# Kernel tuning notes

Measured on AMD Instinct MI355X. Metric: run time of the kernel, lower is better.

## Reference

```python
import jax, jax.numpy as jnp
import numpy as np

B, S, D_MODEL, D_QK = 4, 4096, 256, 64


def setup_inputs() -> dict:
    key = jax.random.key(0)
    ks = jax.random.split(key, 6)
    enc_q = jax.random.normal(ks[0], (B, S, D_MODEL), dtype=jnp.float32)
    enc_k = jax.random.normal(ks[1], (B, S, D_MODEL), dtype=jnp.float32)
    enc_v = jax.random.normal(ks[2], (B, S, D_MODEL), dtype=jnp.float32)
    # torch nn.Linear weight layout: [out_features, in_features]
    Wq = jax.random.normal(ks[3], (D_QK, D_MODEL), dtype=jnp.float32) * (D_MODEL ** -0.5)
    Wk = jax.random.normal(ks[4], (D_QK, D_MODEL), dtype=jnp.float32) * (D_MODEL ** -0.5)
    Wv = jax.random.normal(ks[5], (D_MODEL, D_MODEL), dtype=jnp.float32) * (D_MODEL ** -0.5)
    # causal mask: True above the diagonal -> masked out (matches masked_fill semantics)
    mask = jnp.triu(jnp.ones((S, S), dtype=jnp.bool_), k=1)
    return {"encodings_for_q": enc_q, "encodings_for_k": enc_k,
            "encodings_for_v": enc_v, "mask": mask,
            "Wq": Wq, "Wk": Wk, "Wv": Wv}


def reference(encodings_for_q, encodings_for_k, encodings_for_v, mask, Wq, Wk, Wv):
    # linear projections (no bias): x @ W.T
    q = jnp.einsum('bsd,qd->bsq', encodings_for_q, Wq)   # [B,S,d_qk]
    k = jnp.einsum('bsd,qd->bsq', encodings_for_k, Wk)   # [B,S,d_qk]
    v = jnp.einsum('bsd,ed->bse', encodings_for_v, Wv)   # [B,S,d_model]
    scale = k.shape[-1] ** 0.5                            # sqrt(d_qk)
    sims = jnp.einsum('bsq,btq->bst', q, k) / scale       # [B,S,S]
    sims = jnp.where(mask, jnp.float32(-1e9), sims)
    attn = jax.nn.softmax(sims, axis=-1)
    return jnp.einsum('bst,bte->bse', attn, v)            # [B,S,d_model]
```

## Files before the change

kernel.cpp:

```cpp
#include <hip/hip_runtime.h>


#define BATCH 4
#define SEQ   4096
#define DM    256
#define DQK   64

typedef __bf16 bf16x8 __attribute__((ext_vector_type(8)));
typedef float  f32x16 __attribute__((ext_vector_type(16)));

__device__ __forceinline__ unsigned int rnd16(unsigned int u) {
    return u + 0x7fffu + ((u >> 16) & 1u);
}
__device__ __forceinline__ unsigned short f2bf(float f) {
    return (unsigned short)(rnd16(__builtin_bit_cast(unsigned int, f)) >> 16);
}
__device__ __forceinline__ unsigned int pk2bf(float lo, float hi) {
    unsigned int a = rnd16(__builtin_bit_cast(unsigned int, lo));
    unsigned int b = rnd16(__builtin_bit_cast(unsigned int, hi));
    return (a >> 16) | (b & 0xffff0000u);
}
__device__ __forceinline__ bf16x8 u4bf(uint4 u) { return __builtin_bit_cast(bf16x8, u); }

__device__ __forceinline__ void repack_store(const f32x16& acc, int q2, int l,
                                             uint4* __restrict__ out, size_t tile_ofs_u4) {
    unsigned int d0[4], d1[4], p0[4], p1[4];
#pragma unroll
    for (int h = 0; h < 4; ++h) {
        d0[h] = pk2bf(acc[4*h + 0], acc[4*h + 1]);
        d1[h] = pk2bf(acc[4*h + 2], acc[4*h + 3]);
        p0[h] = __shfl_xor((int)d0[h], 32);
        p1[h] = __shfl_xor((int)d1[h], 32);
    }
#pragma unroll
    for (int kc = 0; kc < 2; ++kc) {
        int h = 2*kc + q2;
        uint4 v = (q2 == 0) ? make_uint4(d0[h], d1[h], p0[h], p1[h])
                            : make_uint4(p0[h], p1[h], d0[h], d1[h]);
        out[tile_ofs_u4 + (size_t)kc * 64 + l] = v;
    }
}

__global__ __launch_bounds__(256) void proj(const float* __restrict__ Xq,
                                            const float* __restrict__ Xk,
                                            const float* __restrict__ Xv,
                                            const float* __restrict__ Wq,
                                            const float* __restrict__ Wk,
                                            const float* __restrict__ Wv,
                                            uint4* __restrict__ qf,
                                            uint4* __restrict__ kf,
                                            uint4* __restrict__ vf) {
    __shared__ unsigned short Xs[64][264];
    __shared__ unsigned short Ws[64][264];

    const int z = blockIdx.z;
    const int bx = blockIdx.x, b = blockIdx.y;
    const float* X = (z == 0) ? Xq : (z == 1) ? Xk : Xv;
    const float* W = (z == 0) ? Wq : (z == 1) ? Wk : Wv;
    const int s0 = bx * 64;
    const int tid = threadIdx.x, w = tid >> 6, l = tid & 63, ln = l & 31, q2 = l >> 5;

#pragma unroll
    for (int i = 0; i < 16; ++i) {
        int f = i * 256 + tid;
        int r = f >> 6, c4 = f & 63;
        float4 xv = *(const float4*)&X[((size_t)b * SEQ + s0 + r) * DM + c4 * 4];
        ushort4 h; h.x = f2bf(xv.x); h.y = f2bf(xv.y); h.z = f2bf(xv.z); h.w = f2bf(xv.w);
        *(ushort4*)&Xs[r][c4 * 4] = h;
    }

    if (z < 2) {
#pragma unroll
        for (int i = 0; i < 16; ++i) {
            int f = i * 256 + tid;
            int r = f >> 6, c4 = f & 63;
            float4 wv = *(const float4*)&W[(size_t)r * DM + c4 * 4];
            ushort4 h; h.x = f2bf(wv.x); h.y = f2bf(wv.y); h.z = f2bf(wv.z); h.w = f2bf(wv.w);
            *(ushort4*)&Ws[r][c4 * 4] = h;
        }
        __syncthreads();
        const int msub = w >> 1, nsub = w & 1;
        f32x16 a0 = {}, a1 = {};
#pragma unroll
        for (int c = 0; c < 16; c += 2) {
            bf16x8 af0 = u4bf(*(const uint4*)&Ws[msub*32 + ln][c*16 + q2*8]);
            bf16x8 bf0 = u4bf(*(const uint4*)&Xs[nsub*32 + ln][c*16 + q2*8]);
            a0 = __builtin_amdgcn_mfma_f32_32x32x16_bf16(af0, bf0, a0, 0, 0, 0);
            bf16x8 af1 = u4bf(*(const uint4*)&Ws[msub*32 + ln][(c+1)*16 + q2*8]);
            bf16x8 bf1 = u4bf(*(const uint4*)&Xs[nsub*32 + ln][(c+1)*16 + q2*8]);
            a1 = __builtin_amdgcn_mfma_f32_32x32x16_bf16(af1, bf1, a1, 0, 0, 0);
        }
        f32x16 acc = a0 + a1;
        size_t base = (((size_t)(b*128 + bx*2 + nsub)) * 4 + 2*msub) * 64;
        repack_store(acc, q2, l, (z == 0) ? qf : kf, base);
    } else {
        const int msub = w & 1, nsub = w >> 1;
        for (int ec = 0; ec < 4; ++ec) {
            __syncthreads();
#pragma unroll
            for (int i = 0; i < 16; ++i) {
                int f = i * 256 + tid;
                int r = f >> 6, c4 = f & 63;
                float4 wv = *(const float4*)&W[(size_t)(ec*64 + r) * DM + c4 * 4];
                ushort4 h; h.x = f2bf(wv.x); h.y = f2bf(wv.y); h.z = f2bf(wv.z); h.w = f2bf(wv.w);
                *(ushort4*)&Ws[r][c4 * 4] = h;
            }
            __syncthreads();
            f32x16 a0 = {}, a1 = {};
#pragma unroll
            for (int c = 0; c < 16; c += 2) {
                bf16x8 af0 = u4bf(*(const uint4*)&Xs[msub*32 + ln][c*16 + q2*8]);
                bf16x8 bf0 = u4bf(*(const uint4*)&Ws[nsub*32 + ln][c*16 + q2*8]);
                a0 = __builtin_amdgcn_mfma_f32_32x32x16_bf16(af0, bf0, a0, 0, 0, 0);
                bf16x8 af1 = u4bf(*(const uint4*)&Xs[msub*32 + ln][(c+1)*16 + q2*8]);
                bf16x8 bf1 = u4bf(*(const uint4*)&Ws[nsub*32 + ln][(c+1)*16 + q2*8]);
                a1 = __builtin_amdgcn_mfma_f32_32x32x16_bf16(af1, bf1, a1, 0, 0, 0);
            }
            f32x16 acc = a0 + a1;
            int et = ec*2 + nsub;
            size_t base = (((size_t)(b*8 + et)) * 256 + (size_t)bx*4 + msub*2) * 64;
            repack_store(acc, q2, l, vf, base);
        }
    }
}

__global__ __launch_bounds__(512) void attn(const uint4* __restrict__ qf,
                                            const uint4* __restrict__ kf,
                                            const uint4* __restrict__ vf,
                                            float* __restrict__ out,
                                            unsigned short* __restrict__ Op,
                                            float* __restrict__ Dp) {
    __shared__ uint4 Pb[2][4][8][64];
    __shared__ float denp[8][2][64];
    __shared__ float dfin[128];

    const int bid = blockIdx.x;
    const int slot = bid & 7, u = bid >> 3;
    const int b = slot >> 1;
    const int task = u * 2 + (slot & 1);
    int T, cc, nc;
    if (task < 12)      { T = task;                cc = 0;             nc = 1; }
    else if (task < 36) { int q = task - 12; T = 12 + (q >> 1); cc = q & 1;     nc = 2; }
    else                { int q = task - 36; T = 24 + q / 3;    cc = q - 3*(q/3); nc = 3; }
    const int n = T + 1;
    const int j0 = cc * n / nc, j1 = (cc + 1) * n / nc;

    const int tid = threadIdx.x, w = tid >> 6, l = tid & 63, ln = l & 31, q2 = l >> 5;
    const int ks = w & 3, qp = w >> 2;
    const float cfac = 0.18033688011112042f;

    bf16x8 qv[2][4];
#pragma unroll
    for (int g = 0; g < 2; ++g)
#pragma unroll
        for (int c = 0; c < 4; ++c)
            qv[g][c] = u4bf(qf[(((size_t)b*128 + T*4 + qp*2 + g) * 4 + c) * 64 + l]);

    f32x16 oa[4] = {};
    float den[2] = {0.f, 0.f};

    uint4 kaf[4];
#pragma unroll
    for (int c = 0; c < 4; ++c)
        kaf[c] = kf[(((size_t)b*128 + j0*4 + ks) * 4 + c) * 64 + l];

    for (int jt = j0; jt < j1; ++jt) {
        const int buf = jt & 1;
        const bool diag = (jt == T);
        f32x16 s0 = {}, s1 = {};
#pragma unroll
        for (int c = 0; c < 4; ++c) {
            bf16x8 ka = u4bf(kaf[c]);
            s0 = __builtin_amdgcn_mfma_f32_32x32x16_bf16(ka, qv[0][c], s0, 0, 0, 0);
            s1 = __builtin_amdgcn_mfma_f32_32x32x16_bf16(ka, qv[1][c], s1, 0, 0, 0);
        }
#pragma unroll
        for (int g = 0; g < 2; ++g) {
            const f32x16 s = g ? s1 : s0;
            const int qsub = qp*2 + g;
            float pv[16], pd = 0.f;
#pragma unroll
            for (int r = 0; r < 16; ++r) {
                float e = __builtin_exp2f(s[r] * cfac);
                if (diag) {
                    int klocal = 4*q2 + (r & 3) + 8*(r >> 2);
                    if (ks*32 + klocal > qsub*32 + ln) e = 0.f;
                }
                pv[r] = e; pd += e;
            }
            den[g] += pd;
#pragma unroll
            for (int quad = 0; quad < 4; ++quad) {
                unsigned int lo = pk2bf(pv[4*quad + 0], pv[4*quad + 1]);
                unsigned int hi = pk2bf(pv[4*quad + 2], pv[4*quad + 3]);
                int kcg = ks*2 + (quad >> 1);
                int h   = quad & 1;
                char* dst = (char*)&Pb[buf][qsub][kcg][h*32 + ln] + q2*8;
                *(uint2*)dst = make_uint2(lo, hi);
            }
        }
        __syncthreads();
        if (jt + 1 < j1) {
#pragma unroll
            for (int c = 0; c < 4; ++c)
                kaf[c] = kf[(((size_t)b*128 + (jt+1)*4 + ks) * 4 + c) * 64 + l];
        }
#pragma unroll
        for (int kc = 0; kc < 8; ++kc) {
            bf16x8 vb = u4bf(vf[(((size_t)b*8 + w) * 256 + jt*8 + kc) * 64 + l]);
#pragma unroll
            for (int qs = 0; qs < 4; ++qs) {
                bf16x8 pa = u4bf(Pb[buf][qs][kc][l]);
                oa[qs] = __builtin_amdgcn_mfma_f32_32x32x16_bf16(pa, vb, oa[qs], 0, 0, 0);
            }
        }
    }

    denp[w][0][l] = den[0];
    denp[w][1][l] = den[1];
    __syncthreads();
    if (tid < 128) {
        int qsub = tid >> 5, qln = tid & 31;
        int g = qsub & 1, wp = qsub >> 1;
        float sden = 0.f;
#pragma unroll
        for (int k4 = 0; k4 < 4; ++k4)
#pragma unroll
            for (int hh = 0; hh < 2; ++hh)
                sden += denp[wp*4 + k4][g][hh*32 + qln];
        dfin[tid] = (nc == 1) ? 1.0f / sden : sden;
    }
    __syncthreads();

    if (nc == 1) {
#pragma unroll
        for (int qs = 0; qs < 4; ++qs)
#pragma unroll
            for (int r = 0; r < 16; ++r) {
                int qrow = qs*32 + (r & 3) + 8*(r >> 2) + 4*q2;
                out[((size_t)b*SEQ + T*128 + qrow) * DM + w*32 + ln] = oa[qs][r] * dfin[qrow];
            }
    } else {
        size_t pidx = (size_t)(b*20 + (T - 12)) * 3 + cc;
#pragma unroll
        for (int qs = 0; qs < 4; ++qs)
#pragma unroll
            for (int r = 0; r < 16; ++r) {
                int qrow = qs*32 + (r & 3) + 8*(r >> 2) + 4*q2;
                Op[(pidx*128 + qrow) * DM + w*32 + ln] = f2bf(oa[qs][r]);
            }
        if (tid < 128) Dp[pidx*128 + tid] = dfin[tid];
    }
}

__global__ __launch_bounds__(256) void combine(const unsigned short* __restrict__ Op,
                                               const float* __restrict__ Dp,
                                               float* __restrict__ out) {
    const int T = 12 + blockIdx.x, b = blockIdx.y, qq = blockIdx.z;
    const int nc = (T < 24) ? 2 : 3;
    const int t = threadIdx.x;
    const size_t base_p = (size_t)(b*20 + (T - 12)) * 3;
#pragma unroll 4
    for (int r = 0; r < 32; ++r) {
        int q = qq*32 + r;
        float sum = 0.f, den = 0.f;
        for (int c = 0; c < nc; ++c) {
            size_t pidx = base_p + c;
            unsigned int uv = Op[(pidx*128 + q) * DM + t];
            sum += __builtin_bit_cast(float, uv << 16);
            den += Dp[pidx*128 + q];
        }
        out[((size_t)b*SEQ + T*128 + q) * DM + t] = sum / den;
    }
}

extern "C" void kernel_launch(void* const* d_in, const int* in_sizes, int n_in,
                              void* d_out, int out_size, void* d_ws, size_t ws_size,
                              hipStream_t stream) {
    const float* enc_q = (const float*)d_in[0];
    const float* enc_k = (const float*)d_in[1];
    const float* enc_v = (const float*)d_in[2];
    const float* Wq = (const float*)d_in[4];
    const float* Wk = (const float*)d_in[5];
    const float* Wv = (const float*)d_in[6];
    float* out = (float*)d_out;

    uint4* qf = (uint4*)d_ws;
    uint4* kf = qf + 131072;
    uint4* vf = kf + 131072;
    unsigned short* Op = (unsigned short*)(vf + 524288);
    float* Dp = (float*)(Op + (size_t)4*20*3*128*256);

    proj<<<dim3(64, 4, 3), 256, 0, stream>>>(enc_q, enc_k, enc_v, Wq, Wk, Wv, qf, kf, vf);
    attn<<<240, 512, 0, stream>>>(qf, kf, vf, out, Op, Dp);
    combine<<<dim3(20, 4, 4), 256, 0, stream>>>(Op, Dp, out);
}
```

Before: 220.5 us.

## Rebalance causal attention split-K with atomics and split V projection across blocks

The causal attention work split is rebalanced so that tile T is divided into T/5+1 key chunks, giving 488 blocks instead of 240. Split partial results are accumulated directly into the output and a denominator buffer with float atomics, replacing the bf16 partial buffer and combine kernel with memsets plus a lightweight normalization pass. The V projection is also split across two grid z-slices, and attn gains an occupancy hint. The trade-off is atomic traffic and memset overhead, and the summation order is now nondeterministic.

```diff
diff --git a/kernel.cpp b/kernel.cpp
--- a/kernel.cpp
+++ b/kernel.cpp
@@ -95,7 +95,8 @@
         repack_store(acc, q2, l, (z == 0) ? qf : kf, base);
     } else {
         const int msub = w & 1, nsub = w >> 1;
-        for (int ec = 0; ec < 4; ++ec) {
+        for (int ecl = 0; ecl < 2; ++ecl) {
+            const int ec = (z - 2) * 2 + ecl;
             __syncthreads();
 #pragma unroll
             for (int i = 0; i < 16; ++i) {
@@ -124,24 +125,25 @@
     }
 }
 
-__global__ __launch_bounds__(512) void attn(const uint4* __restrict__ qf,
-                                            const uint4* __restrict__ kf,
-                                            const uint4* __restrict__ vf,
-                                            float* __restrict__ out,
-                                            unsigned short* __restrict__ Op,
-                                            float* __restrict__ Dp) {
+__global__ __launch_bounds__(512, 4) void attn(const uint4* __restrict__ qf,
+                                               const uint4* __restrict__ kf,
+                                               const uint4* __restrict__ vf,
+                                               float* __restrict__ out,
+                                               float* __restrict__ deng) {
     __shared__ uint4 Pb[2][4][8][64];
     __shared__ float denp[8][2][64];
     __shared__ float dfin[128];
 
     const int bid = blockIdx.x;
     const int slot = bid & 7, u = bid >> 3;
-    const int b = slot >> 1;
-    const int task = u * 2 + (slot & 1);
-    int T, cc, nc;
-    if (task < 12)      { T = task;                cc = 0;             nc = 1; }
-    else if (task < 36) { int q = task - 12; T = 12 + (q >> 1); cc = q & 1;     nc = 2; }
-    else                { int q = task - 36; T = 24 + q / 3;    cc = q - 3*(q/3); nc = 3; }
+    const int b = slot >> 1, par = slot & 1;
+    int T = -1, cc = 0, nc = 1, acc_t = 0;
+    for (int t = par; t < 32; t += 2) {
+        int n_t = t / 5 + 1;
+        if (u < acc_t + n_t) { T = t; cc = u - acc_t; nc = n_t; break; }
+        acc_t += n_t;
+    }
+    if (T < 0) return;
     const int n = T + 1;
     const int j0 = cc * n / nc, j1 = (cc + 1) * n / nc;
 
@@ -241,36 +243,30 @@
                 out[((size_t)b*SEQ + T*128 + qrow) * DM + w*32 + ln] = oa[qs][r] * dfin[qrow];
             }
     } else {
-        size_t pidx = (size_t)(b*20 + (T - 12)) * 3 + cc;
 #pragma unroll
         for (int qs = 0; qs < 4; ++qs)
 #pragma unroll
             for (int r = 0; r < 16; ++r) {
                 int qrow = qs*32 + (r & 3) + 8*(r >> 2) + 4*q2;
-                Op[(pidx*128 + qrow) * DM + w*32 + ln] = f2bf(oa[qs][r]);
-            }
-        if (tid < 128) Dp[pidx*128 + tid] = dfin[tid];
-    }
-}
-
-__global__ __launch_bounds__(256) void combine(const unsigned short* __restrict__ Op,
-                                               const float* __restrict__ Dp,
-                                               float* __restrict__ out) {
-    const int T = 12 + blockIdx.x, b = blockIdx.y, qq = blockIdx.z;
-    const int nc = (T < 24) ? 2 : 3;
-    const int t = threadIdx.x;
-    const size_t base_p = (size_t)(b*20 + (T - 12)) * 3;
-#pragma unroll 4
-    for (int r = 0; r < 32; ++r) {
-        int q = qq*32 + r;
-        float sum = 0.f, den = 0.f;
-        for (int c = 0; c < nc; ++c) {
-            size_t pidx = base_p + c;
-            unsigned int uv = Op[(pidx*128 + q) * DM + t];
-            sum += __builtin_bit_cast(float, uv << 16);
-            den += Dp[pidx*128 + q];
-        }
-        out[((size_t)b*SEQ + T*128 + q) * DM + t] = sum / den;
+                atomicAdd(&out[((size_t)b*SEQ + T*128 + qrow) * DM + w*32 + ln], oa[qs][r]);
+            }
+        if (tid < 128) atomicAdd(&deng[(size_t)(b*32 + T)*128 + tid], dfin[tid]);
+    }
+}
+
+__global__ __launch_bounds__(256) void norm_split(float* __restrict__ out,
+                                                  const float* __restrict__ deng) {
+    const int b = blockIdx.y;
+    const int s0 = 640 + blockIdx.x * 16;
+    const int tid = threadIdx.x;
+#pragma unroll
+    for (int g = 0; g < 4; ++g) {
+        int s = s0 + g*4 + (tid >> 6);
+        float inv = 1.0f / deng[(size_t)(b*32 + (s >> 7))*128 + (s & 127)];
+        float4* p = (float4*)&out[((size_t)b*SEQ + s) * DM] + (tid & 63);
+        float4 v = *p;
+        v.x *= inv; v.y *= inv; v.z *= inv; v.w *= inv;
+        *p = v;
     }
 }
 
@@ -288,10 +284,14 @@
     uint4* qf = (uint4*)d_ws;
     uint4* kf = qf + 131072;
     uint4* vf = kf + 131072;
-    unsigned short* Op = (unsigned short*)(vf + 524288);
-    float* Dp = (float*)(Op + (size_t)4*20*3*128*256);
-
-    proj<<<dim3(64, 4, 3), 256, 0, stream>>>(enc_q, enc_k, enc_v, Wq, Wk, Wv, qf, kf, vf);
-    attn<<<240, 512, 0, stream>>>(qf, kf, vf, out, Op, Dp);
-    combine<<<dim3(20, 4, 4), 256, 0, stream>>>(Op, Dp, out);
-}
+    float* deng = (float*)(vf + 524288);
+
+    for (int b = 0; b < BATCH; ++b)
+        hipMemsetAsync(out + ((size_t)b * SEQ + 640) * DM, 0,
+                       (size_t)(SEQ - 640) * DM * sizeof(float), stream);
+    hipMemsetAsync(deng, 0, (size_t)BATCH * 32 * 128 * sizeof(float), stream);
+
+    proj<<<dim3(64, 4, 4), 256, 0, stream>>>(enc_q, enc_k, enc_v, Wq, Wk, Wv, qf, kf, vf);
+    attn<<<488, 512, 0, stream>>>(qf, kf, vf, out, deng);
+    norm_split<<<dim3(216, 4), 256, 0, stream>>>(out, deng);
+}
```

Measured after the change: 256.2 us. 16.2% more time.

## Software-pipeline attention loop and split V projection across two grid slices

Applied to the files above, without the earlier changes.

Restructures the attention inner loop so each iteration runs the P·V MFMAs for the previous key tile before computing scores for the current tile, with a peeled prologue and epilogue. This lets QK^T/softmax work overlap the PV matrix work and hides the K load latency behind the PV MFMAs. The V projection is split across two z-slices (grid z goes from 3 to 4), giving more parallelism in proj. The partial-output buffer is also compacted with a slot_base index.

```diff
diff --git a/kernel.cpp b/kernel.cpp
--- a/kernel.cpp
+++ b/kernel.cpp
@@ -95,7 +95,8 @@
         repack_store(acc, q2, l, (z == 0) ? qf : kf, base);
     } else {
         const int msub = w & 1, nsub = w >> 1;
-        for (int ec = 0; ec < 4; ++ec) {
+        for (int ecl = 0; ecl < 2; ++ecl) {
+            const int ec = (z - 2) * 2 + ecl;
             __syncthreads();
 #pragma unroll
             for (int i = 0; i < 16; ++i) {
@@ -122,6 +123,10 @@
             repack_store(acc, q2, l, vf, base);
         }
     }
+}
+
+__device__ __forceinline__ int slot_base(int T) {
+    return (T < 24) ? (T - 12) * 2 : 24 + (T - 24) * 3;
 }
 
 __global__ __launch_bounds__(512) void attn(const uint4* __restrict__ qf,
@@ -139,8 +144,8 @@
     const int b = slot >> 1;
     const int task = u * 2 + (slot & 1);
     int T, cc, nc;
-    if (task < 12)      { T = task;                cc = 0;             nc = 1; }
-    else if (task < 36) { int q = task - 12; T = 12 + (q >> 1); cc = q & 1;     nc = 2; }
+    if (task < 12)      { T = task;                cc = 0;               nc = 1; }
+    else if (task < 36) { int q = task - 12; T = 12 + (q >> 1); cc = q & 1;       nc = 2; }
     else                { int q = task - 36; T = 24 + q / 3;    cc = q - 3*(q/3); nc = 3; }
     const int n = T + 1;
     const int j0 = cc * n / nc, j1 = (cc + 1) * n / nc;
@@ -159,21 +164,15 @@
     f32x16 oa[4] = {};
     float den[2] = {0.f, 0.f};
 
-    uint4 kaf[4];
-#pragma unroll
-    for (int c = 0; c < 4; ++c)
-        kaf[c] = kf[(((size_t)b*128 + j0*4 + ks) * 4 + c) * 64 + l];
-
-    for (int jt = j0; jt < j1; ++jt) {
-        const int buf = jt & 1;
-        const bool diag = (jt == T);
+    {
         f32x16 s0 = {}, s1 = {};
 #pragma unroll
         for (int c = 0; c < 4; ++c) {
-            bf16x8 ka = u4bf(kaf[c]);
+            bf16x8 ka = u4bf(kf[(((size_t)b*128 + j0*4 + ks) * 4 + c) * 64 + l]);
             s0 = __builtin_amdgcn_mfma_f32_32x32x16_bf16(ka, qv[0][c], s0, 0, 0, 0);
             s1 = __builtin_amdgcn_mfma_f32_32x32x16_bf16(ka, qv[1][c], s1, 0, 0, 0);
         }
+        const bool diag = (j0 == T);
 #pragma unroll
         for (int g = 0; g < 2; ++g) {
             const f32x16 s = g ? s1 : s0;
@@ -195,22 +194,75 @@
                 unsigned int hi = pk2bf(pv[4*quad + 2], pv[4*quad + 3]);
                 int kcg = ks*2 + (quad >> 1);
                 int h   = quad & 1;
-                char* dst = (char*)&Pb[buf][qsub][kcg][h*32 + ln] + q2*8;
+                char* dst = (char*)&Pb[j0 & 1][qsub][kcg][h*32 + ln] + q2*8;
                 *(uint2*)dst = make_uint2(lo, hi);
             }
         }
         __syncthreads();
-        if (jt + 1 < j1) {
-#pragma unroll
-            for (int c = 0; c < 4; ++c)
-                kaf[c] = kf[(((size_t)b*128 + (jt+1)*4 + ks) * 4 + c) * 64 + l];
-        }
+    }
+
+    for (int jt = j0 + 1; jt < j1; ++jt) {
+        uint4 kaf[4];
+#pragma unroll
+        for (int c = 0; c < 4; ++c)
+            kaf[c] = kf[(((size_t)b*128 + jt*4 + ks) * 4 + c) * 64 + l];
+
+        const int pbuf = (jt - 1) & 1;
 #pragma unroll
         for (int kc = 0; kc < 8; ++kc) {
-            bf16x8 vb = u4bf(vf[(((size_t)b*8 + w) * 256 + jt*8 + kc) * 64 + l]);
+            bf16x8 vb = u4bf(vf[(((size_t)b*8 + w) * 256 + (size_t)(jt-1)*8 + kc) * 64 + l]);
 #pragma unroll
             for (int qs = 0; qs < 4; ++qs) {
-                bf16x8 pa = u4bf(Pb[buf][qs][kc][l]);
+                bf16x8 pa = u4bf(Pb[pbuf][qs][kc][l]);
+                oa[qs] = __builtin_amdgcn_mfma_f32_32x32x16_bf16(pa, vb, oa[qs], 0, 0, 0);
+            }
+        }
+
+        f32x16 s0 = {}, s1 = {};
+#pragma unroll
+        for (int c = 0; c < 4; ++c) {
+            bf16x8 ka = u4bf(kaf[c]);
+            s0 = __builtin_amdgcn_mfma_f32_32x32x16_bf16(ka, qv[0][c], s0, 0, 0, 0);
+            s1 = __builtin_amdgcn_mfma_f32_32x32x16_bf16(ka, qv[1][c], s1, 0, 0, 0);
+        }
+
+        const bool diag = (jt == T);
+#pragma unroll
+        for (int g = 0; g < 2; ++g) {
+            const f32x16 s = g ? s1 : s0;
+            const int qsub = qp*2 + g;
+            float pv[16], pd = 0.f;
+#pragma unroll
+            for (int r = 0; r < 16; ++r) {
+                float e = __builtin_exp2f(s[r] * cfac);
+                if (diag) {
+                    int klocal = 4*q2 + (r & 3) + 8*(r >> 2);
+                    if (ks*32 + klocal > qsub*32 + ln) e = 0.f;
+                }
+                pv[r] = e; pd += e;
+            }
+            den[g] += pd;
+#pragma unroll
+            for (int quad = 0; quad < 4; ++quad) {
+                unsigned int lo = pk2bf(pv[4*quad + 0], pv[4*quad + 1]);
+                unsigned int hi = pk2bf(pv[4*quad + 2], pv[4*quad + 3]);
+                int kcg = ks*2 + (quad >> 1);
+                int h   = quad & 1;
+                char* dst = (char*)&Pb[jt & 1][qsub][kcg][h*32 + ln] + q2*8;
+                *(uint2*)dst = make_uint2(lo, hi);
+            }
+        }
+        __syncthreads();
+    }
+
+    {
+        const int pbuf = (j1 - 1) & 1;
+#pragma unroll
+        for (int kc = 0; kc < 8; ++kc) {
+            bf16x8 vb = u4bf(vf[(((size_t)b*8 + w) * 256 + (size_t)(j1-1)*8 + kc) * 64 + l]);
+#pragma unroll
+            for (int qs = 0; qs < 4; ++qs) {
+                bf16x8 pa = u4bf(Pb[pbuf][qs][kc][l]);
                 oa[qs] = __builtin_amdgcn_mfma_f32_32x32x16_bf16(pa, vb, oa[qs], 0, 0, 0);
             }
         }
@@ -241,7 +293,7 @@
                 out[((size_t)b*SEQ + T*128 + qrow) * DM + w*32 + ln] = oa[qs][r] * dfin[qrow];
             }
     } else {
-        size_t pidx = (size_t)(b*20 + (T - 12)) * 3 + cc;
+        size_t pidx = (size_t)b*48 + slot_base(T) + cc;
 #pragma unroll
         for (int qs = 0; qs < 4; ++qs)
 #pragma unroll
@@ -259,7 +311,7 @@
     const int T = 12 + blockIdx.x, b = blockIdx.y, qq = blockIdx.z;
     const int nc = (T < 24) ? 2 : 3;
     const int t = threadIdx.x;
-    const size_t base_p = (size_t)(b*20 + (T - 12)) * 3;
+    const size_t base_p = (size_t)b*48 + slot_base(T);
 #pragma unroll 4
     for (int r = 0; r < 32; ++r) {
         int q = qq*32 + r;
@@ -289,9 +341,9 @@
     uint4* kf = qf + 131072;
     uint4* vf = kf + 131072;
     unsigned short* Op = (unsigned short*)(vf + 524288);
-    float* Dp = (float*)(Op + (size_t)4*20*3*128*256);
-
-    proj<<<dim3(64, 4, 3), 256, 0, stream>>>(enc_q, enc_k, enc_v, Wq, Wk, Wv, qf, kf, vf);
+    float* Dp = (float*)(Op + (size_t)4*48*128*256);
+
+    proj<<<dim3(64, 4, 4), 256, 0, stream>>>(enc_q, enc_k, enc_v, Wq, Wk, Wv, qf, kf, vf);
     attn<<<240, 512, 0, stream>>>(qf, kf, vf, out, Op, Dp);
     combine<<<dim3(20, 4, 4), 256, 0, stream>>>(Op, Dp, out);
 }
```

Result: slower. 225.8 us (+2.4%).

## Rebalance causal attention split-K chunking and split V projection across two z-slices

Applied to the files above, without the earlier changes.

Attention tasks are now assigned with a finer split-K schedule in which row tile T gets T/6+1 chunks, giving 102 tasks per batch (408 blocks) instead of 60. The first chunk writes its unnormalized fp32 output straight into out, and only the remaining chunks go to bf16 partial buffers, which combine then adds in. The V projection is split over two grid z-slices so each block does half the output columns, and attn gains a min-blocks launch bound. The aim is better load balance and CU fill, at the cost of more combine work, more partial-buffer traffic, and tighter register limits.

```diff
diff --git a/kernel.cpp b/kernel.cpp
--- a/kernel.cpp
+++ b/kernel.cpp
@@ -39,6 +39,11 @@
                             : make_uint4(p0[h], p1[h], d0[h], d1[h]);
         out[tile_ofs_u4 + (size_t)kc * 64 + l] = v;
     }
+}
+
+__device__ __forceinline__ int obase(int T) {
+    int g = T / 6;
+    return 3*g*(g-1) + (T - 6*g)*g;
 }
 
 __global__ __launch_bounds__(256) void proj(const float* __restrict__ Xq,
@@ -95,7 +100,8 @@
         repack_store(acc, q2, l, (z == 0) ? qf : kf, base);
     } else {
         const int msub = w & 1, nsub = w >> 1;
-        for (int ec = 0; ec < 4; ++ec) {
+        for (int ecl = 0; ecl < 2; ++ecl) {
+            const int ec = (z - 2) * 2 + ecl;
             __syncthreads();
 #pragma unroll
             for (int i = 0; i < 16; ++i) {
@@ -124,12 +130,12 @@
     }
 }
 
-__global__ __launch_bounds__(512) void attn(const uint4* __restrict__ qf,
-                                            const uint4* __restrict__ kf,
-                                            const uint4* __restrict__ vf,
-                                            float* __restrict__ out,
-                                            unsigned short* __restrict__ Op,
-                                            float* __restrict__ Dp) {
+__global__ __launch_bounds__(512, 4) void attn(const uint4* __restrict__ qf,
+                                               const uint4* __restrict__ kf,
+                                               const uint4* __restrict__ vf,
+                                               float* __restrict__ out,
+                                               unsigned short* __restrict__ Op,
+                                               float* __restrict__ Dp) {
     __shared__ uint4 Pb[2][4][8][64];
     __shared__ float denp[8][2][64];
     __shared__ float dfin[128];
@@ -138,10 +144,12 @@
     const int slot = bid & 7, u = bid >> 3;
     const int b = slot >> 1;
     const int task = u * 2 + (slot & 1);
-    int T, cc, nc;
-    if (task < 12)      { T = task;                cc = 0;             nc = 1; }
-    else if (task < 36) { int q = task - 12; T = 12 + (q >> 1); cc = q & 1;     nc = 2; }
-    else                { int q = task - 36; T = 24 + q / 3;    cc = q - 3*(q/3); nc = 3; }
+    int T = 0, cc = 0, nc = 1, acc_t = 0;
+    for (int t = 0; t < 32; ++t) {
+        int n_t = t / 6 + 1;
+        if (task < acc_t + n_t) { T = t; cc = task - acc_t; nc = n_t; break; }
+        acc_t += n_t;
+    }
     const int n = T + 1;
     const int j0 = cc * n / nc, j1 = (cc + 1) * n / nc;
 
@@ -207,7 +215,7 @@
         }
 #pragma unroll
         for (int kc = 0; kc < 8; ++kc) {
-            bf16x8 vb = u4bf(vf[(((size_t)b*8 + w) * 256 + jt*8 + kc) * 64 + l]);
+            bf16x8 vb = u4bf(vf[(((size_t)b*8 + w) * 256 + (size_t)jt*8 + kc) * 64 + l]);
 #pragma unroll
             for (int qs = 0; qs < 4; ++qs) {
                 bf16x8 pa = u4bf(Pb[buf][qs][kc][l]);
@@ -240,8 +248,17 @@
                 int qrow = qs*32 + (r & 3) + 8*(r >> 2) + 4*q2;
                 out[((size_t)b*SEQ + T*128 + qrow) * DM + w*32 + ln] = oa[qs][r] * dfin[qrow];
             }
+    } else if (cc == 0) {
+#pragma unroll
+        for (int qs = 0; qs < 4; ++qs)
+#pragma unroll
+            for (int r = 0; r < 16; ++r) {
+                int qrow = qs*32 + (r & 3) + 8*(r >> 2) + 4*q2;
+                out[((size_t)b*SEQ + T*128 + qrow) * DM + w*32 + ln] = oa[qs][r];
+            }
+        if (tid < 128) Dp[((size_t)b*96 + obase(T) + (T - 6)) * 128 + tid] = dfin[tid];
     } else {
-        size_t pidx = (size_t)(b*20 + (T - 12)) * 3 + cc;
+        size_t pidx = (size_t)b*70 + obase(T) + (cc - 1);
 #pragma unroll
         for (int qs = 0; qs < 4; ++qs)
 #pragma unroll
@@ -249,28 +266,31 @@
                 int qrow = qs*32 + (r & 3) + 8*(r >> 2) + 4*q2;
                 Op[(pidx*128 + qrow) * DM + w*32 + ln] = f2bf(oa[qs][r]);
             }
-        if (tid < 128) Dp[pidx*128 + tid] = dfin[tid];
+        if (tid < 128) Dp[((size_t)b*96 + obase(T) + (T - 6) + cc) * 128 + tid] = dfin[tid];
     }
 }
 
 __global__ __launch_bounds__(256) void combine(const unsigned short* __restrict__ Op,
                                                const float* __restrict__ Dp,
                                                float* __restrict__ out) {
-    const int T = 12 + blockIdx.x, b = blockIdx.y, qq = blockIdx.z;
-    const int nc = (T < 24) ? 2 : 3;
+    const int T = 6 + blockIdx.x, b = blockIdx.y, qq = blockIdx.z;
+    const int nc = T / 6 + 1;
     const int t = threadIdx.x;
-    const size_t base_p = (size_t)(b*20 + (T - 12)) * 3;
+    const int ob = obase(T);
+    const size_t dbase = (size_t)b*96 + ob + (T - 6);
+    const size_t pbase = (size_t)b*70 + ob;
 #pragma unroll 4
     for (int r = 0; r < 32; ++r) {
         int q = qq*32 + r;
-        float sum = 0.f, den = 0.f;
-        for (int c = 0; c < nc; ++c) {
-            size_t pidx = base_p + c;
-            unsigned int uv = Op[(pidx*128 + q) * DM + t];
+        size_t oofs = ((size_t)b*SEQ + T*128 + q) * DM + t;
+        float sum = out[oofs];
+        float dsum = 0.f;
+        for (int c = 0; c < nc; ++c) dsum += Dp[(dbase + c)*128 + q];
+        for (int c = 1; c < nc; ++c) {
+            unsigned int uv = Op[((pbase + c - 1)*128 + q) * DM + t];
             sum += __builtin_bit_cast(float, uv << 16);
-            den += Dp[pidx*128 + q];
-        }
-        out[((size_t)b*SEQ + T*128 + q) * DM + t] = sum / den;
+        }
+        out[oofs] = sum / dsum;
     }
 }
 
@@ -289,9 +309,9 @@
     uint4* kf = qf + 131072;
     uint4* vf = kf + 131072;
     unsigned short* Op = (unsigned short*)(vf + 524288);
-    float* Dp = (float*)(Op + (size_t)4*20*3*128*256);
-
-    proj<<<dim3(64, 4, 3), 256, 0, stream>>>(enc_q, enc_k, enc_v, Wq, Wk, Wv, qf, kf, vf);
-    attn<<<240, 512, 0, stream>>>(qf, kf, vf, out, Op, Dp);
-    combine<<<dim3(20, 4, 4), 256, 0, stream>>>(Op, Dp, out);
-}
+    float* Dp = (float*)(Op + (size_t)4*70*128*256);
+
+    proj<<<dim3(64, 4, 4), 256, 0, stream>>>(enc_q, enc_k, enc_v, Wq, Wk, Wv, qf, kf, vf);
+    attn<<<408, 512, 0, stream>>>(qf, kf, vf, out, Op, Dp);
+    combine<<<dim3(26, 4, 4), 256, 0, stream>>>(Op, Dp, out);
+}
```

Measured after the change: 265.4 us. 1.2x slower.
